# Performance work log

Measured on AMD Instinct MI355X. Metric: run time of the kernel, lower is better.

## Reference

```python
import jax, jax.numpy as jnp
import numpy as np

D_MODEL = 1024
N_HEADS = 16
HEAD_DIM = D_MODEL // N_HEADS


def setup_inputs() -> dict:
    key = jax.random.key(0)
    ks = jax.random.split(key, 9)
    B, S = 2, 2048
    s = 1.0 / np.sqrt(D_MODEL)
    x = jax.random.normal(ks[0], (B, S, D_MODEL), dtype=jnp.float32)
    Wq = jax.random.normal(ks[1], (N_HEADS, D_MODEL, HEAD_DIM), dtype=jnp.float32) * s
    Wk = jax.random.normal(ks[2], (N_HEADS, D_MODEL, HEAD_DIM), dtype=jnp.float32) * s
    Wv = jax.random.normal(ks[3], (N_HEADS, D_MODEL, HEAD_DIM), dtype=jnp.float32) * s
    bq = jax.random.normal(ks[4], (N_HEADS, HEAD_DIM), dtype=jnp.float32) * s
    bk = jax.random.normal(ks[5], (N_HEADS, HEAD_DIM), dtype=jnp.float32) * s
    bv = jax.random.normal(ks[6], (N_HEADS, HEAD_DIM), dtype=jnp.float32) * s
    Wp = jax.random.normal(ks[7], (D_MODEL, D_MODEL), dtype=jnp.float32) * s
    bp = jax.random.normal(ks[8], (D_MODEL,), dtype=jnp.float32) * s
    return {"x": x, "Wq": Wq, "Wk": Wk, "Wv": Wv, "bq": bq, "bk": bk, "bv": bv, "Wp": Wp, "bp": bp}


def reference(x, Wq, Wk, Wv, bq, bk, bv, Wp, bp):
    # Per-head projections batched over heads: [B,S,D] x [H,D,E] -> [B,H,S,E]
    Q = jnp.einsum('bsd,hde->bhse', x, Wq) + bq[None, :, None, :]
    K = jnp.einsum('bsd,hde->bhse', x, Wk) + bk[None, :, None, :]
    V = jnp.einsum('bsd,hde->bhse', x, Wv) + bv[None, :, None, :]
    scores = jnp.einsum('bhse,bhte->bhst', Q, K) / jnp.sqrt(jnp.asarray(HEAD_DIM, x.dtype))
    attn = jax.nn.softmax(scores, axis=-1)          # [B,H,S,S]
    out = jnp.einsum('bhst,bhte->bhse', attn, V)    # [B,H,S,E]
    B, H, S, E = out.shape
    concat = out.transpose(0, 2, 1, 3).reshape(B, S, H * E)  # concat heads along feature
    return concat @ Wp.T + bp
```

## Files before the change

### kernel.cpp

```cpp
#include <hip/hip_runtime.h>
#include <hip/hip_bf16.h>

typedef __attribute__((ext_vector_type(8))) short short8;
typedef __attribute__((ext_vector_type(4))) float float4_t;

#define D_MODEL 1024
#define N_HEADS 16
#define HEAD_DIM 64
#define B_SZ 2
#define SEQ 2048
#define M_ROWS (B_SZ*SEQ)
#define NQKV 3072
#define SC_LOG2E 0.18033688011112042f

__device__ __forceinline__ unsigned short f2bf(float f) {
  unsigned u = __float_as_uint(f);
  u += 0x7FFFu + ((u >> 16) & 1u);
  return (unsigned short)(u >> 16);
}

__device__ __forceinline__ void gl_lds16(const unsigned short* g, unsigned short* l) {
  __builtin_amdgcn_global_load_lds(
      (const __attribute__((address_space(1))) unsigned int*)(size_t)g,
      (__attribute__((address_space(3))) unsigned int*)(unsigned int)(size_t)l,
      16, 0, 0);
}

__global__ void prep(const float* __restrict__ x, const float* __restrict__ Wp,
                     const float* __restrict__ Wq, const float* __restrict__ Wk,
                     const float* __restrict__ Wv,
                     unsigned short* __restrict__ xb, unsigned short* __restrict__ Wpb,
                     unsigned short* __restrict__ Wall) {
  __shared__ float t[16][17];
  int bid = blockIdx.x;
  if (bid < 5120) {
    const float* src; unsigned short* dst; int base;
    if (bid < 4096) { src = x;  dst = xb;  base = bid * 1024 + threadIdx.x * 4; }
    else            { src = Wp; dst = Wpb; base = (bid - 4096) * 1024 + threadIdx.x * 4; }
    float4 v = *(const float4*)(src + base);
    dst[base + 0] = f2bf(v.x);
    dst[base + 1] = f2bf(v.y);
    dst[base + 2] = f2bf(v.z);
    dst[base + 3] = f2bf(v.w);
  } else {
    int u = bid - 5120;
    int sel = u >> 12;
    u &= 4095;
    const float* W = sel == 0 ? Wq : (sel == 1 ? Wk : Wv);
    int d0 = (u & 63) * 16, e0 = ((u >> 6) & 3) * 16, hh = u >> 8;
    int tx = threadIdx.x & 15, ty = threadIdx.x >> 4;
    t[ty][tx] = W[hh * (D_MODEL * HEAD_DIM) + (d0 + ty) * HEAD_DIM + e0 + tx];
    __syncthreads();
    Wall[(size_t)(sel * 1024 + hh * 64 + e0 + ty) * D_MODEL + d0 + tx] = f2bf(t[tx][ty]);
  }
}

__global__ __launch_bounds__(256) void qkv_gemm(const unsigned short* __restrict__ xb,
                                                const unsigned short* __restrict__ Wall,
                                                const float* __restrict__ bq,
                                                const float* __restrict__ bk,
                                                const float* __restrict__ bv,
                                                unsigned short* __restrict__ Qb,
                                                unsigned short* __restrict__ Kb,
                                                unsigned short* __restrict__ Vtb) {
  __shared__ unsigned short As[128 * 32], Bs[128 * 32];
  __shared__ __align__(16) unsigned short Vstage[4][16 * 72];
  const int m0 = blockIdx.x * 128, n0 = blockIdx.y * 128;
  const int lane = threadIdx.x & 63, w = threadIdx.x >> 6;
  const int l16 = lane & 15, quad = lane >> 4;
  const int wm = w & 1, wn = w >> 1;
  const int ldrow = lane >> 2, ldcol = (lane & 3) * 8;
  const unsigned short* ga0 = xb + (size_t)(m0 + w * 32 + ldrow) * D_MODEL + ldcol;
  const unsigned short* ga1 = ga0 + 16 * D_MODEL;
  const unsigned short* gb0 = Wall + (size_t)(n0 + w * 32 + ldrow) * D_MODEL + ldcol;
  const unsigned short* gb1 = gb0 + 16 * D_MODEL;
  unsigned short* lA0 = As + (w * 2 + 0) * 512;
  unsigned short* lA1 = As + (w * 2 + 1) * 512;
  unsigned short* lB0 = Bs + (w * 2 + 0) * 512;
  unsigned short* lB1 = Bs + (w * 2 + 1) * 512;
  float4_t acc[4][4];
  float4_t z = {0.f, 0.f, 0.f, 0.f};
#pragma unroll
  for (int i = 0; i < 4; i++)
#pragma unroll
    for (int j = 0; j < 4; j++) acc[i][j] = z;
  for (int k0 = 0; k0 < D_MODEL; k0 += 32) {
    __syncthreads();
    gl_lds16(ga0 + k0, lA0);
    gl_lds16(ga1 + k0, lA1);
    gl_lds16(gb0 + k0, lB0);
    gl_lds16(gb1 + k0, lB1);
    __syncthreads();
    short8 af[4], bf[4];
#pragma unroll
    for (int i = 0; i < 4; i++) af[i] = *(const short8*)&As[(wm * 64 + i * 16 + l16) * 32 + quad * 8];
#pragma unroll
    for (int j = 0; j < 4; j++) bf[j] = *(const short8*)&Bs[(wn * 64 + j * 16 + l16) * 32 + quad * 8];
#pragma unroll
    for (int i = 0; i < 4; i++)
#pragma unroll
      for (int j = 0; j < 4; j++)
        acc[i][j] = __builtin_amdgcn_mfma_f32_16x16x32_bf16(af[i], bf[j], acc[i][j], 0, 0, 0);
  }
  const int nb = n0 + wn * 64;
  const int sel = nb >> 10;
  const int h = (nb >> 6) & 15;
  const float* bias = sel == 0 ? bq : (sel == 1 ? bk : bv);
  if (sel == 2) {
    unsigned short* vs = &Vstage[w][0];
    const int mbase = m0 + wm * 64;
    const int bb = mbase >> 11;
    const size_t vbase = (size_t)(bb * N_HEADS + h) * (32 * 4096) +
                         (size_t)((mbase >> 6) & 31) * 4096;
    const int e8 = lane >> 3, ch = lane & 7;
#pragma unroll
    for (int j = 0; j < 4; j++) {
      float be = bias[h * 64 + j * 16 + l16];
#pragma unroll
      for (int i = 0; i < 4; i++)
#pragma unroll
        for (int r = 0; r < 4; r++)
          vs[l16 * 72 + i * 16 + quad * 4 + r] = f2bf(acc[i][j][r] + be);
#pragma unroll
      for (int rd = 0; rd < 2; rd++) {
        int er = rd * 8 + e8;
        short8 val = *(const short8*)(vs + er * 72 + ch * 8);
        *(short8*)(Vtb + vbase + (size_t)(j * 16 + er) * 64 + ch * 8) = val;
      }
    }
  } else {
#pragma unroll
    for (int i = 0; i < 4; i++) {
#pragma unroll
      for (int j = 0; j < 4; j++) {
#pragma unroll
        for (int r = 0; r < 4; r++) {
          int m = m0 + wm * 64 + i * 16 + quad * 4 + r;
          int e = j * 16 + l16;
          int bb = m >> 11, s = m & (SEQ - 1);
          size_t bh = (size_t)(bb * N_HEADS + h);
          float v = acc[i][j][r] + bias[h * 64 + e];
          if (sel == 0) Qb[(bh * SEQ + s) * HEAD_DIM + e] = f2bf(v * SC_LOG2E);
          else          Kb[(bh * SEQ + s) * HEAD_DIM + e] = f2bf(v);
        }
      }
    }
  }
}

__global__ __launch_bounds__(256) void attn_kernel(const unsigned short* __restrict__ Q,
                                                   const unsigned short* __restrict__ K,
                                                   const unsigned short* __restrict__ Vt,
                                                   unsigned short* __restrict__ concat) {
  __shared__ __align__(16) unsigned short Ks0[64 * 72], Ks1[64 * 72];
  __shared__ __align__(16) unsigned short Vs0[64 * 72], Vs1[64 * 72];
  __shared__ __align__(16) unsigned short Ps[4][32 * 72];
  const int b = blockIdx.z, h = blockIdx.y;
  const int lane = threadIdx.x & 63, w = threadIdx.x >> 6;
  const int l16 = lane & 15, quad = lane >> 4;
  const size_t bh = (size_t)(b * N_HEADS + h);
  const int q0 = blockIdx.x * 128 + w * 32;
  float4_t z = {0.f, 0.f, 0.f, 0.f};

  short8 aq[2][2];
#pragma unroll
  for (int rg = 0; rg < 2; rg++)
#pragma unroll
    for (int hf = 0; hf < 2; hf++)
      aq[rg][hf] = *(const short8*)(Q + (bh * SEQ + q0 + rg * 16 + l16) * HEAD_DIM + hf * 32 + quad * 8);

  const int srow = lane >> 3, schk = lane & 7;
  const unsigned short* kg = K + (bh * SEQ + w * 16 + srow) * HEAD_DIM + schk * 8;
  const unsigned short* vg = Vt + bh * (32 * 4096) + (w * 16 + srow) * 64 + schk * 8;
  const int tl0 = w * 16 + srow, tl1 = tl0 + 8;
  const int kwr0 = (((tl0 >> 1) & 15) | ((tl0 & 1) << 4) | (tl0 & 32)) * 72 + schk * 8;
  const int kwr1 = (((tl1 >> 1) & 15) | ((tl1 & 1) << 4) | (tl1 & 32)) * 72 + schk * 8;
  const int vwr0 = (w * 16 + srow) * 72 + schk * 8;
  const int vwr1 = vwr0 + 8 * 72;

  float4_t o[2][4];
  float4_t ls[2] = {z, z};
#pragma unroll
  for (int rg = 0; rg < 2; rg++)
#pragma unroll
    for (int ne = 0; ne < 4; ne++) o[rg][ne] = z;
  short8 ones;
#pragma unroll
  for (int i = 0; i < 8; i++) ones[i] = (short)0x3F80;
  unsigned short* pb = &Ps[w][0];

  short8 kreg0 = *(const short8*)kg;
  short8 kreg1 = *(const short8*)(kg + 512);
  short8 vreg0 = *(const short8*)vg;
  short8 vreg1 = *(const short8*)(vg + 512);
  kg += 4096; vg += 4096;

  auto step = [&](unsigned short* kb, unsigned short* vb, int itv) {
    *(short8*)(kb + kwr0) = kreg0;
    *(short8*)(kb + kwr1) = kreg1;
    *(short8*)(vb + vwr0) = vreg0;
    *(short8*)(vb + vwr1) = vreg1;
    __syncthreads();
    if (itv < 31) {
      kreg0 = *(const short8*)kg;
      kreg1 = *(const short8*)(kg + 512);
      vreg0 = *(const short8*)vg;
      vreg1 = *(const short8*)(vg + 512);
      kg += 4096; vg += 4096;
    }
    float4_t s[2][4];
#pragma unroll
    for (int nt = 0; nt < 4; nt++) {
      short8 k0 = *(const short8*)(kb + (nt * 16 + l16) * 72 + quad * 8);
      short8 k1 = *(const short8*)(kb + (nt * 16 + l16) * 72 + 32 + quad * 8);
      s[0][nt] = __builtin_amdgcn_mfma_f32_16x16x32_bf16(aq[0][0], k0, z, 0, 0, 0);
      s[0][nt] = __builtin_amdgcn_mfma_f32_16x16x32_bf16(aq[0][1], k1, s[0][nt], 0, 0, 0);
      s[1][nt] = __builtin_amdgcn_mfma_f32_16x16x32_bf16(aq[1][0], k0, z, 0, 0, 0);
      s[1][nt] = __builtin_amdgcn_mfma_f32_16x16x32_bf16(aq[1][1], k1, s[1][nt], 0, 0, 0);
    }
#pragma unroll
    for (int rg = 0; rg < 2; rg++) {
#pragma unroll
      for (int r = 0; r < 4; r++) {
        int row = rg * 16 + quad * 4 + r;
        float p0 = __builtin_amdgcn_exp2f(s[rg][0][r]);
        float p1 = __builtin_amdgcn_exp2f(s[rg][1][r]);
        __hip_bfloat162 pp = __float22bfloat162_rn(float2{p0, p1});
        *(unsigned int*)(pb + row * 72 + 2 * l16) = *(unsigned int*)&pp;
        float p2 = __builtin_amdgcn_exp2f(s[rg][2][r]);
        float p3 = __builtin_amdgcn_exp2f(s[rg][3][r]);
        __hip_bfloat162 qq = __float22bfloat162_rn(float2{p2, p3});
        *(unsigned int*)(pb + row * 72 + 32 + 2 * l16) = *(unsigned int*)&qq;
      }
    }
    short8 pa[2][2];
#pragma unroll
    for (int rg = 0; rg < 2; rg++)
#pragma unroll
      for (int hf = 0; hf < 2; hf++)
        pa[rg][hf] = *(const short8*)(pb + (rg * 16 + l16) * 72 + hf * 32 + quad * 8);
#pragma unroll
    for (int rg = 0; rg < 2; rg++) {
      ls[rg] = __builtin_amdgcn_mfma_f32_16x16x32_bf16(pa[rg][0], ones, ls[rg], 0, 0, 0);
      ls[rg] = __builtin_amdgcn_mfma_f32_16x16x32_bf16(pa[rg][1], ones, ls[rg], 0, 0, 0);
    }
#pragma unroll
    for (int ne = 0; ne < 4; ne++) {
#pragma unroll
      for (int hf = 0; hf < 2; hf++) {
        short8 vf = *(const short8*)(vb + (ne * 16 + l16) * 72 + hf * 32 + quad * 8);
        o[0][ne] = __builtin_amdgcn_mfma_f32_16x16x32_bf16(pa[0][hf], vf, o[0][ne], 0, 0, 0);
        o[1][ne] = __builtin_amdgcn_mfma_f32_16x16x32_bf16(pa[1][hf], vf, o[1][ne], 0, 0, 0);
      }
    }
  };

  for (int it2 = 0; it2 < 16; ++it2) {
    step(Ks0, Vs0, 2 * it2);
    step(Ks1, Vs1, 2 * it2 + 1);
  }

#pragma unroll
  for (int rg = 0; rg < 2; rg++) {
#pragma unroll
    for (int r = 0; r < 4; r++) {
      float li = 1.0f / ls[rg][r];
      int sr = q0 + rg * 16 + quad * 4 + r;
#pragma unroll
      for (int ne = 0; ne < 4; ne++)
        concat[((size_t)(b * SEQ + sr)) * D_MODEL + h * 64 + ne * 16 + l16] = f2bf(o[rg][ne][r] * li);
    }
  }
}

__global__ __launch_bounds__(256) void out_gemm(const unsigned short* __restrict__ cb,
                                                const unsigned short* __restrict__ Wpb,
                                                const float* __restrict__ bp,
                                                float* __restrict__ out) {
  __shared__ unsigned short As[128 * 32], Bs[128 * 32];
  const int m0 = blockIdx.x * 128, n0 = blockIdx.y * 128;
  const int lane = threadIdx.x & 63, w = threadIdx.x >> 6;
  const int l16 = lane & 15, quad = lane >> 4;
  const int wm = w & 1, wn = w >> 1;
  const int ldrow = lane >> 2, ldcol = (lane & 3) * 8;
  const unsigned short* ga0 = cb + (size_t)(m0 + w * 32 + ldrow) * D_MODEL + ldcol;
  const unsigned short* ga1 = ga0 + 16 * D_MODEL;
  const unsigned short* gb0 = Wpb + (size_t)(n0 + w * 32 + ldrow) * D_MODEL + ldcol;
  const unsigned short* gb1 = gb0 + 16 * D_MODEL;
  unsigned short* lA0 = As + (w * 2 + 0) * 512;
  unsigned short* lA1 = As + (w * 2 + 1) * 512;
  unsigned short* lB0 = Bs + (w * 2 + 0) * 512;
  unsigned short* lB1 = Bs + (w * 2 + 1) * 512;
  float4_t acc[4][4];
  float4_t z = {0.f, 0.f, 0.f, 0.f};
#pragma unroll
  for (int i = 0; i < 4; i++)
#pragma unroll
    for (int j = 0; j < 4; j++) acc[i][j] = z;
  for (int k0 = 0; k0 < D_MODEL; k0 += 32) {
    __syncthreads();
    gl_lds16(ga0 + k0, lA0);
    gl_lds16(ga1 + k0, lA1);
    gl_lds16(gb0 + k0, lB0);
    gl_lds16(gb1 + k0, lB1);
    __syncthreads();
    short8 af[4], bf[4];
#pragma unroll
    for (int i = 0; i < 4; i++) af[i] = *(const short8*)&As[(wm * 64 + i * 16 + l16) * 32 + quad * 8];
#pragma unroll
    for (int j = 0; j < 4; j++) bf[j] = *(const short8*)&Bs[(wn * 64 + j * 16 + l16) * 32 + quad * 8];
#pragma unroll
    for (int i = 0; i < 4; i++)
#pragma unroll
      for (int j = 0; j < 4; j++)
        acc[i][j] = __builtin_amdgcn_mfma_f32_16x16x32_bf16(af[i], bf[j], acc[i][j], 0, 0, 0);
  }
#pragma unroll
  for (int i = 0; i < 4; i++)
#pragma unroll
    for (int j = 0; j < 4; j++)
#pragma unroll
      for (int r = 0; r < 4; r++) {
        int m = m0 + wm * 64 + i * 16 + quad * 4 + r;
        int oc = n0 + wn * 64 + j * 16 + l16;
        out[(size_t)m * D_MODEL + oc] = acc[i][j][r] + bp[oc];
      }
}

extern "C" void kernel_launch(void* const* d_in, const int* in_sizes, int n_in,
                              void* d_out, int out_size, void* d_ws, size_t ws_size,
                              hipStream_t stream) {
  const float* x  = (const float*)d_in[0];
  const float* Wq = (const float*)d_in[1];
  const float* Wk = (const float*)d_in[2];
  const float* Wv = (const float*)d_in[3];
  const float* bq = (const float*)d_in[4];
  const float* bk = (const float*)d_in[5];
  const float* bv = (const float*)d_in[6];
  const float* Wp = (const float*)d_in[7];
  const float* bp = (const float*)d_in[8];
  float* out = (float*)d_out;

  char* ws = (char*)d_ws;
  size_t off = 0;
  auto alloc = [&](size_t bytes) -> void* {
    void* p = ws + off;
    off += (bytes + 255) & ~(size_t)255;
    return p;
  };
  unsigned short* xb   = (unsigned short*)alloc((size_t)M_ROWS * D_MODEL * 2);
  unsigned short* Wall = (unsigned short*)alloc((size_t)NQKV * D_MODEL * 2);
  unsigned short* Wpb  = (unsigned short*)alloc((size_t)D_MODEL * D_MODEL * 2);
  unsigned short* Qb   = (unsigned short*)alloc((size_t)B_SZ * N_HEADS * SEQ * HEAD_DIM * 2);
  unsigned short* Kb   = (unsigned short*)alloc((size_t)B_SZ * N_HEADS * SEQ * HEAD_DIM * 2);
  unsigned short* Vtb  = (unsigned short*)alloc((size_t)B_SZ * N_HEADS * SEQ * HEAD_DIM * 2);
  unsigned short* cbuf = (unsigned short*)alloc((size_t)B_SZ * SEQ * D_MODEL * 2);

  prep<<<17408, 256, 0, stream>>>(x, Wp, Wq, Wk, Wv, xb, Wpb, Wall);

  qkv_gemm<<<dim3(M_ROWS / 128, NQKV / 128), 256, 0, stream>>>(xb, Wall, bq, bk, bv, Qb, Kb, Vtb);

  attn_kernel<<<dim3(SEQ / 128, N_HEADS, B_SZ), 256, 0, stream>>>(Qb, Kb, Vtb, cbuf);

  out_gemm<<<dim3(M_ROWS / 128, D_MODEL / 128), 256, 0, stream>>>(cbuf, Wpb, bp, out);
}
```

Before: 207.3 us.

## Halve attention query tile per wave and stage Q/K stores through LDS

The attention kernel now gives each wave 16 query rows instead of 32 and launches twice as many blocks (64 queries per block). This raises grid parallelism and cuts register pressure, at the cost of loading each K/V tile into LDS twice as often. The QKV GEMM epilogue for Q and K now transposes through a small LDS stage so each lane writes 16-byte vectors instead of scattered 2-byte stores. That gives coalesced output writes in exchange for extra LDS traffic.

```diff
diff --git a/kernel.cpp b/kernel.cpp
--- a/kernel.cpp
+++ b/kernel.cpp
@@ -64,7 +64,7 @@
                                                 unsigned short* __restrict__ Kb,
                                                 unsigned short* __restrict__ Vtb) {
   __shared__ unsigned short As[128 * 32], Bs[128 * 32];
-  __shared__ __align__(16) unsigned short Vstage[4][16 * 72];
+  __shared__ __align__(16) unsigned short Stage[4][16 * 72];
   const int m0 = blockIdx.x * 128, n0 = blockIdx.y * 128;
   const int lane = threadIdx.x & 63, w = threadIdx.x >> 6;
   const int l16 = lane & 15, quad = lane >> 4;
@@ -106,12 +106,12 @@
   const int sel = nb >> 10;
   const int h = (nb >> 6) & 15;
   const float* bias = sel == 0 ? bq : (sel == 1 ? bk : bv);
+  const int mbase = m0 + wm * 64;
+  const int bb = mbase >> 11;
+  const size_t bh = (size_t)(bb * N_HEADS + h);
   if (sel == 2) {
-    unsigned short* vs = &Vstage[w][0];
-    const int mbase = m0 + wm * 64;
-    const int bb = mbase >> 11;
-    const size_t vbase = (size_t)(bb * N_HEADS + h) * (32 * 4096) +
-                         (size_t)((mbase >> 6) & 31) * 4096;
+    unsigned short* vs = &Stage[w][0];
+    const size_t vbase = bh * (32 * 4096) + (size_t)((mbase >> 6) & 31) * 4096;
     const int e8 = lane >> 3, ch = lane & 7;
 #pragma unroll
     for (int j = 0; j < 4; j++) {
@@ -129,20 +129,24 @@
       }
     }
   } else {
-#pragma unroll
-    for (int i = 0; i < 4; i++) {
-#pragma unroll
-      for (int j = 0; j < 4; j++) {
-#pragma unroll
-        for (int r = 0; r < 4; r++) {
-          int m = m0 + wm * 64 + i * 16 + quad * 4 + r;
-          int e = j * 16 + l16;
-          int bb = m >> 11, s = m & (SEQ - 1);
-          size_t bh = (size_t)(bb * N_HEADS + h);
-          float v = acc[i][j][r] + bias[h * 64 + e];
-          if (sel == 0) Qb[(bh * SEQ + s) * HEAD_DIM + e] = f2bf(v * SC_LOG2E);
-          else          Kb[(bh * SEQ + s) * HEAD_DIM + e] = f2bf(v);
-        }
+    unsigned short* st = &Stage[w][0];
+    unsigned short* dst = (sel == 0) ? Qb : Kb;
+    const float qsc = (sel == 0) ? SC_LOG2E : 1.0f;
+    const size_t rowbase = bh * SEQ + (mbase & (SEQ - 1));
+    const int r2 = lane >> 1, c2 = lane & 1;
+#pragma unroll
+    for (int j = 0; j < 4; j++) {
+      float be = bias[h * 64 + j * 16 + l16];
+#pragma unroll
+      for (int i = 0; i < 4; i++)
+#pragma unroll
+        for (int r = 0; r < 4; r++)
+          st[(i * 16 + quad * 4 + r) * 18 + l16] = f2bf((acc[i][j][r] + be) * qsc);
+#pragma unroll
+      for (int p = 0; p < 2; p++) {
+        int row = p * 32 + r2;
+        short8 val = *(const short8*)(st + row * 18 + c2 * 8);
+        *(short8*)(dst + (rowbase + row) * HEAD_DIM + j * 16 + c2 * 8) = val;
       }
     }
   }
@@ -154,20 +158,16 @@
                                                    unsigned short* __restrict__ concat) {
   __shared__ __align__(16) unsigned short Ks0[64 * 72], Ks1[64 * 72];
   __shared__ __align__(16) unsigned short Vs0[64 * 72], Vs1[64 * 72];
-  __shared__ __align__(16) unsigned short Ps[4][32 * 72];
+  __shared__ __align__(16) unsigned short Ps[4][16 * 72];
   const int b = blockIdx.z, h = blockIdx.y;
   const int lane = threadIdx.x & 63, w = threadIdx.x >> 6;
   const int l16 = lane & 15, quad = lane >> 4;
   const size_t bh = (size_t)(b * N_HEADS + h);
-  const int q0 = blockIdx.x * 128 + w * 32;
+  const int q0 = blockIdx.x * 64 + w * 16;
   float4_t z = {0.f, 0.f, 0.f, 0.f};
 
-  short8 aq[2][2];
-#pragma unroll
-  for (int rg = 0; rg < 2; rg++)
-#pragma unroll
-    for (int hf = 0; hf < 2; hf++)
-      aq[rg][hf] = *(const short8*)(Q + (bh * SEQ + q0 + rg * 16 + l16) * HEAD_DIM + hf * 32 + quad * 8);
+  short8 aq0 = *(const short8*)(Q + (bh * SEQ + q0 + l16) * HEAD_DIM + quad * 8);
+  short8 aq1 = *(const short8*)(Q + (bh * SEQ + q0 + l16) * HEAD_DIM + 32 + quad * 8);
 
   const int srow = lane >> 3, schk = lane & 7;
   const unsigned short* kg = K + (bh * SEQ + w * 16 + srow) * HEAD_DIM + schk * 8;
@@ -178,12 +178,8 @@
   const int vwr0 = (w * 16 + srow) * 72 + schk * 8;
   const int vwr1 = vwr0 + 8 * 72;
 
-  float4_t o[2][4];
-  float4_t ls[2] = {z, z};
-#pragma unroll
-  for (int rg = 0; rg < 2; rg++)
-#pragma unroll
-    for (int ne = 0; ne < 4; ne++) o[rg][ne] = z;
+  float4_t o[4] = {z, z, z, z};
+  float4_t ls = z;
   short8 ones;
 #pragma unroll
   for (int i = 0; i < 8; i++) ones[i] = (short)0x3F80;
@@ -208,50 +204,36 @@
       vreg1 = *(const short8*)(vg + 512);
       kg += 4096; vg += 4096;
     }
-    float4_t s[2][4];
+    float4_t s[4];
 #pragma unroll
     for (int nt = 0; nt < 4; nt++) {
       short8 k0 = *(const short8*)(kb + (nt * 16 + l16) * 72 + quad * 8);
       short8 k1 = *(const short8*)(kb + (nt * 16 + l16) * 72 + 32 + quad * 8);
-      s[0][nt] = __builtin_amdgcn_mfma_f32_16x16x32_bf16(aq[0][0], k0, z, 0, 0, 0);
-      s[0][nt] = __builtin_amdgcn_mfma_f32_16x16x32_bf16(aq[0][1], k1, s[0][nt], 0, 0, 0);
-      s[1][nt] = __builtin_amdgcn_mfma_f32_16x16x32_bf16(aq[1][0], k0, z, 0, 0, 0);
-      s[1][nt] = __builtin_amdgcn_mfma_f32_16x16x32_bf16(aq[1][1], k1, s[1][nt], 0, 0, 0);
-    }
-#pragma unroll
-    for (int rg = 0; rg < 2; rg++) {
-#pragma unroll
-      for (int r = 0; r < 4; r++) {
-        int row = rg * 16 + quad * 4 + r;
-        float p0 = __builtin_amdgcn_exp2f(s[rg][0][r]);
-        float p1 = __builtin_amdgcn_exp2f(s[rg][1][r]);
-        __hip_bfloat162 pp = __float22bfloat162_rn(float2{p0, p1});
-        *(unsigned int*)(pb + row * 72 + 2 * l16) = *(unsigned int*)&pp;
-        float p2 = __builtin_amdgcn_exp2f(s[rg][2][r]);
-        float p3 = __builtin_amdgcn_exp2f(s[rg][3][r]);
-        __hip_bfloat162 qq = __float22bfloat162_rn(float2{p2, p3});
-        *(unsigned int*)(pb + row * 72 + 32 + 2 * l16) = *(unsigned int*)&qq;
-      }
-    }
-    short8 pa[2][2];
-#pragma unroll
-    for (int rg = 0; rg < 2; rg++)
-#pragma unroll
-      for (int hf = 0; hf < 2; hf++)
-        pa[rg][hf] = *(const short8*)(pb + (rg * 16 + l16) * 72 + hf * 32 + quad * 8);
-#pragma unroll
-    for (int rg = 0; rg < 2; rg++) {
-      ls[rg] = __builtin_amdgcn_mfma_f32_16x16x32_bf16(pa[rg][0], ones, ls[rg], 0, 0, 0);
-      ls[rg] = __builtin_amdgcn_mfma_f32_16x16x32_bf16(pa[rg][1], ones, ls[rg], 0, 0, 0);
-    }
+      s[nt] = __builtin_amdgcn_mfma_f32_16x16x32_bf16(aq0, k0, z, 0, 0, 0);
+      s[nt] = __builtin_amdgcn_mfma_f32_16x16x32_bf16(aq1, k1, s[nt], 0, 0, 0);
+    }
+#pragma unroll
+    for (int r = 0; r < 4; r++) {
+      int row = quad * 4 + r;
+      float p0 = __builtin_amdgcn_exp2f(s[0][r]);
+      float p1 = __builtin_amdgcn_exp2f(s[1][r]);
+      __hip_bfloat162 pp = __float22bfloat162_rn(float2{p0, p1});
+      *(unsigned int*)(pb + row * 72 + 2 * l16) = *(unsigned int*)&pp;
+      float p2 = __builtin_amdgcn_exp2f(s[2][r]);
+      float p3 = __builtin_amdgcn_exp2f(s[3][r]);
+      __hip_bfloat162 qq = __float22bfloat162_rn(float2{p2, p3});
+      *(unsigned int*)(pb + row * 72 + 32 + 2 * l16) = *(unsigned int*)&qq;
+    }
+    short8 pa0 = *(const short8*)(pb + l16 * 72 + quad * 8);
+    short8 pa1 = *(const short8*)(pb + l16 * 72 + 32 + quad * 8);
+    ls = __builtin_amdgcn_mfma_f32_16x16x32_bf16(pa0, ones, ls, 0, 0, 0);
+    ls = __builtin_amdgcn_mfma_f32_16x16x32_bf16(pa1, ones, ls, 0, 0, 0);
 #pragma unroll
     for (int ne = 0; ne < 4; ne++) {
-#pragma unroll
-      for (int hf = 0; hf < 2; hf++) {
-        short8 vf = *(const short8*)(vb + (ne * 16 + l16) * 72 + hf * 32 + quad * 8);
-        o[0][ne] = __builtin_amdgcn_mfma_f32_16x16x32_bf16(pa[0][hf], vf, o[0][ne], 0, 0, 0);
-        o[1][ne] = __builtin_amdgcn_mfma_f32_16x16x32_bf16(pa[1][hf], vf, o[1][ne], 0, 0, 0);
-      }
+      short8 vf0 = *(const short8*)(vb + (ne * 16 + l16) * 72 + quad * 8);
+      short8 vf1 = *(const short8*)(vb + (ne * 16 + l16) * 72 + 32 + quad * 8);
+      o[ne] = __builtin_amdgcn_mfma_f32_16x16x32_bf16(pa0, vf0, o[ne], 0, 0, 0);
+      o[ne] = __builtin_amdgcn_mfma_f32_16x16x32_bf16(pa1, vf1, o[ne], 0, 0, 0);
     }
   };
 
@@ -261,15 +243,12 @@
   }
 
 #pragma unroll
-  for (int rg = 0; rg < 2; rg++) {
-#pragma unroll
-    for (int r = 0; r < 4; r++) {
-      float li = 1.0f / ls[rg][r];
-      int sr = q0 + rg * 16 + quad * 4 + r;
-#pragma unroll
-      for (int ne = 0; ne < 4; ne++)
-        concat[((size_t)(b * SEQ + sr)) * D_MODEL + h * 64 + ne * 16 + l16] = f2bf(o[rg][ne][r] * li);
-    }
+  for (int r = 0; r < 4; r++) {
+    float li = 1.0f / ls[r];
+    int sr = q0 + quad * 4 + r;
+#pragma unroll
+    for (int ne = 0; ne < 4; ne++)
+      concat[((size_t)(b * SEQ + sr)) * D_MODEL + h * 64 + ne * 16 + l16] = f2bf(o[ne][r] * li);
   }
 }
 
@@ -360,7 +339,7 @@
 
   qkv_gemm<<<dim3(M_ROWS / 128, NQKV / 128), 256, 0, stream>>>(xb, Wall, bq, bk, bv, Qb, Kb, Vtb);
 
-  attn_kernel<<<dim3(SEQ / 128, N_HEADS, B_SZ), 256, 0, stream>>>(Qb, Kb, Vtb, cbuf);
+  attn_kernel<<<dim3(SEQ / 64, N_HEADS, B_SZ), 256, 0, stream>>>(Qb, Kb, Vtb, cbuf);
 
   out_gemm<<<dim3(M_ROWS / 128, D_MODEL / 128), 256, 0, stream>>>(cbuf, Wpb, bp, out);
 }
```

Result: slower. 227.3 us (+9.7%).

## Stage Q/K epilogue stores through LDS, shrink out_gemm N tile, unpad P buffer

Applied to the files above, without the earlier changes.

The Q/K epilogue of the QKV GEMM now writes bias-added bf16 values into a per-wave LDS stage and then issues 16-byte vectorized global stores, replacing scattered 2-byte stores. The output projection GEMM uses a 128x64 tile, which doubles the grid to fill more CUs, with each wave computing 32 rows. The attention P staging buffer drops its row padding from 72 to 64 elements, which saves LDS but may add bank conflicts.

```diff
diff --git a/kernel.cpp b/kernel.cpp
--- a/kernel.cpp
+++ b/kernel.cpp
@@ -64,7 +64,7 @@
                                                 unsigned short* __restrict__ Kb,
                                                 unsigned short* __restrict__ Vtb) {
   __shared__ unsigned short As[128 * 32], Bs[128 * 32];
-  __shared__ __align__(16) unsigned short Vstage[4][16 * 72];
+  __shared__ __align__(16) unsigned short Stage[4][16 * 72];
   const int m0 = blockIdx.x * 128, n0 = blockIdx.y * 128;
   const int lane = threadIdx.x & 63, w = threadIdx.x >> 6;
   const int l16 = lane & 15, quad = lane >> 4;
@@ -106,12 +106,12 @@
   const int sel = nb >> 10;
   const int h = (nb >> 6) & 15;
   const float* bias = sel == 0 ? bq : (sel == 1 ? bk : bv);
+  const int mbase = m0 + wm * 64;
+  const int bb = mbase >> 11;
+  const size_t bh = (size_t)(bb * N_HEADS + h);
   if (sel == 2) {
-    unsigned short* vs = &Vstage[w][0];
-    const int mbase = m0 + wm * 64;
-    const int bb = mbase >> 11;
-    const size_t vbase = (size_t)(bb * N_HEADS + h) * (32 * 4096) +
-                         (size_t)((mbase >> 6) & 31) * 4096;
+    unsigned short* vs = &Stage[w][0];
+    const size_t vbase = bh * (32 * 4096) + (size_t)((mbase >> 6) & 31) * 4096;
     const int e8 = lane >> 3, ch = lane & 7;
 #pragma unroll
     for (int j = 0; j < 4; j++) {
@@ -129,20 +129,24 @@
       }
     }
   } else {
-#pragma unroll
-    for (int i = 0; i < 4; i++) {
-#pragma unroll
-      for (int j = 0; j < 4; j++) {
-#pragma unroll
-        for (int r = 0; r < 4; r++) {
-          int m = m0 + wm * 64 + i * 16 + quad * 4 + r;
-          int e = j * 16 + l16;
-          int bb = m >> 11, s = m & (SEQ - 1);
-          size_t bh = (size_t)(bb * N_HEADS + h);
-          float v = acc[i][j][r] + bias[h * 64 + e];
-          if (sel == 0) Qb[(bh * SEQ + s) * HEAD_DIM + e] = f2bf(v * SC_LOG2E);
-          else          Kb[(bh * SEQ + s) * HEAD_DIM + e] = f2bf(v);
-        }
+    unsigned short* st = &Stage[w][0];
+    unsigned short* dst = (sel == 0) ? Qb : Kb;
+    const float qsc = (sel == 0) ? SC_LOG2E : 1.0f;
+    const size_t rowbase = bh * SEQ + (mbase & (SEQ - 1));
+    const int r2 = lane >> 1, c2 = lane & 1;
+#pragma unroll
+    for (int j = 0; j < 4; j++) {
+      float be = bias[h * 64 + j * 16 + l16];
+#pragma unroll
+      for (int i = 0; i < 4; i++)
+#pragma unroll
+        for (int r = 0; r < 4; r++)
+          st[(i * 16 + quad * 4 + r) * 18 + l16] = f2bf((acc[i][j][r] + be) * qsc);
+#pragma unroll
+      for (int p = 0; p < 2; p++) {
+        int row = p * 32 + r2;
+        short8 val = *(const short8*)(st + row * 18 + c2 * 8);
+        *(short8*)(dst + (rowbase + row) * HEAD_DIM + j * 16 + c2 * 8) = val;
       }
     }
   }
@@ -154,7 +158,7 @@
                                                    unsigned short* __restrict__ concat) {
   __shared__ __align__(16) unsigned short Ks0[64 * 72], Ks1[64 * 72];
   __shared__ __align__(16) unsigned short Vs0[64 * 72], Vs1[64 * 72];
-  __shared__ __align__(16) unsigned short Ps[4][32 * 72];
+  __shared__ __align__(16) unsigned short Ps[4][32 * 64];
   const int b = blockIdx.z, h = blockIdx.y;
   const int lane = threadIdx.x & 63, w = threadIdx.x >> 6;
   const int l16 = lane & 15, quad = lane >> 4;
@@ -226,11 +230,11 @@
         float p0 = __builtin_amdgcn_exp2f(s[rg][0][r]);
         float p1 = __builtin_amdgcn_exp2f(s[rg][1][r]);
         __hip_bfloat162 pp = __float22bfloat162_rn(float2{p0, p1});
-        *(unsigned int*)(pb + row * 72 + 2 * l16) = *(unsigned int*)&pp;
+        *(unsigned int*)(pb + row * 64 + 2 * l16) = *(unsigned int*)&pp;
         float p2 = __builtin_amdgcn_exp2f(s[rg][2][r]);
         float p3 = __builtin_amdgcn_exp2f(s[rg][3][r]);
         __hip_bfloat162 qq = __float22bfloat162_rn(float2{p2, p3});
-        *(unsigned int*)(pb + row * 72 + 32 + 2 * l16) = *(unsigned int*)&qq;
+        *(unsigned int*)(pb + row * 64 + 32 + 2 * l16) = *(unsigned int*)&qq;
       }
     }
     short8 pa[2][2];
@@ -238,7 +242,7 @@
     for (int rg = 0; rg < 2; rg++)
 #pragma unroll
       for (int hf = 0; hf < 2; hf++)
-        pa[rg][hf] = *(const short8*)(pb + (rg * 16 + l16) * 72 + hf * 32 + quad * 8);
+        pa[rg][hf] = *(const short8*)(pb + (rg * 16 + l16) * 64 + hf * 32 + quad * 8);
 #pragma unroll
     for (int rg = 0; rg < 2; rg++) {
       ls[rg] = __builtin_amdgcn_mfma_f32_16x16x32_bf16(pa[rg][0], ones, ls[rg], 0, 0, 0);
@@ -277,24 +281,21 @@
                                                 const unsigned short* __restrict__ Wpb,
                                                 const float* __restrict__ bp,
                                                 float* __restrict__ out) {
-  __shared__ unsigned short As[128 * 32], Bs[128 * 32];
-  const int m0 = blockIdx.x * 128, n0 = blockIdx.y * 128;
+  __shared__ unsigned short As[128 * 32], Bs[64 * 32];
+  const int m0 = blockIdx.x * 128, n0 = blockIdx.y * 64;
   const int lane = threadIdx.x & 63, w = threadIdx.x >> 6;
   const int l16 = lane & 15, quad = lane >> 4;
-  const int wm = w & 1, wn = w >> 1;
   const int ldrow = lane >> 2, ldcol = (lane & 3) * 8;
   const unsigned short* ga0 = cb + (size_t)(m0 + w * 32 + ldrow) * D_MODEL + ldcol;
   const unsigned short* ga1 = ga0 + 16 * D_MODEL;
-  const unsigned short* gb0 = Wpb + (size_t)(n0 + w * 32 + ldrow) * D_MODEL + ldcol;
-  const unsigned short* gb1 = gb0 + 16 * D_MODEL;
+  const unsigned short* gb0 = Wpb + (size_t)(n0 + w * 16 + ldrow) * D_MODEL + ldcol;
   unsigned short* lA0 = As + (w * 2 + 0) * 512;
   unsigned short* lA1 = As + (w * 2 + 1) * 512;
-  unsigned short* lB0 = Bs + (w * 2 + 0) * 512;
-  unsigned short* lB1 = Bs + (w * 2 + 1) * 512;
-  float4_t acc[4][4];
+  unsigned short* lB0 = Bs + w * 512;
+  float4_t acc[2][4];
   float4_t z = {0.f, 0.f, 0.f, 0.f};
 #pragma unroll
-  for (int i = 0; i < 4; i++)
+  for (int i = 0; i < 2; i++)
 #pragma unroll
     for (int j = 0; j < 4; j++) acc[i][j] = z;
   for (int k0 = 0; k0 < D_MODEL; k0 += 32) {
@@ -302,27 +303,26 @@
     gl_lds16(ga0 + k0, lA0);
     gl_lds16(ga1 + k0, lA1);
     gl_lds16(gb0 + k0, lB0);
-    gl_lds16(gb1 + k0, lB1);
-    __syncthreads();
-    short8 af[4], bf[4];
-#pragma unroll
-    for (int i = 0; i < 4; i++) af[i] = *(const short8*)&As[(wm * 64 + i * 16 + l16) * 32 + quad * 8];
-#pragma unroll
-    for (int j = 0; j < 4; j++) bf[j] = *(const short8*)&Bs[(wn * 64 + j * 16 + l16) * 32 + quad * 8];
-#pragma unroll
-    for (int i = 0; i < 4; i++)
+    __syncthreads();
+    short8 af[2], bf[4];
+#pragma unroll
+    for (int i = 0; i < 2; i++) af[i] = *(const short8*)&As[(w * 32 + i * 16 + l16) * 32 + quad * 8];
+#pragma unroll
+    for (int j = 0; j < 4; j++) bf[j] = *(const short8*)&Bs[(j * 16 + l16) * 32 + quad * 8];
+#pragma unroll
+    for (int i = 0; i < 2; i++)
 #pragma unroll
       for (int j = 0; j < 4; j++)
         acc[i][j] = __builtin_amdgcn_mfma_f32_16x16x32_bf16(af[i], bf[j], acc[i][j], 0, 0, 0);
   }
 #pragma unroll
-  for (int i = 0; i < 4; i++)
+  for (int i = 0; i < 2; i++)
 #pragma unroll
     for (int j = 0; j < 4; j++)
 #pragma unroll
       for (int r = 0; r < 4; r++) {
-        int m = m0 + wm * 64 + i * 16 + quad * 4 + r;
-        int oc = n0 + wn * 64 + j * 16 + l16;
+        int m = m0 + w * 32 + i * 16 + quad * 4 + r;
+        int oc = n0 + j * 16 + l16;
         out[(size_t)m * D_MODEL + oc] = acc[i][j][r] + bp[oc];
       }
 }
@@ -362,5 +362,5 @@
 
   attn_kernel<<<dim3(SEQ / 128, N_HEADS, B_SZ), 256, 0, stream>>>(Qb, Kb, Vtb, cbuf);
 
-  out_gemm<<<dim3(M_ROWS / 128, D_MODEL / 128), 256, 0, stream>>>(cbuf, Wpb, bp, out);
-}
+  out_gemm<<<dim3(M_ROWS / 128, D_MODEL / 64), 256, 0, stream>>>(cbuf, Wpb, bp, out);
+}
```

New measurement: 210.1 us. No clear change (+1.3%).
